# Optimization experiments

Measured on AMD Instinct MI355X. Metric: run time of the kernel, lower is better.

## Reference

```python
import jax, jax.numpy as jnp
import numpy as np

B, S, D, H = 4, 2048, 512, 8
EPS = 1e-5

def _layer_norm(x, gamma, beta):
    mu = jnp.mean(x, axis=-1, keepdims=True)
    var = jnp.mean(jnp.square(x - mu), axis=-1, keepdims=True)
    return (x - mu) * jax.lax.rsqrt(var + EPS) * gamma + beta

def setup_inputs() -> dict:
    key = jax.random.key(0)
    ks = jax.random.split(key, 6)
    sc = 1.0 / np.sqrt(D)
    return {
        "seq_k": jax.random.normal(ks[0], (B, S, D), jnp.float32),
        "seq_q": jax.random.normal(ks[1], (B, S, D), jnp.float32),
        "seq_v": jax.random.normal(ks[2], (B, S, D), jnp.float32),
        "W1": jax.random.normal(ks[3], (D, D), jnp.float32) * sc,
        "W2": jax.random.normal(ks[4], (D, D), jnp.float32) * sc,
        "W3": jax.random.normal(ks[5], (D, D), jnp.float32) * sc,
        "gamma": jnp.ones((D,), jnp.float32),
        "beta": jnp.zeros((D,), jnp.float32),
    }

def reference(seq_k, seq_q, seq_v, W1, W2, W3, gamma, beta):
    # is_layer_norm=True: pre-LN on values; seq_v_value is the normed v
    v_in = _layer_norm(seq_v, gamma, beta)
    # nn.Linear(bias=False): y = x @ W^T
    q = seq_q @ W1.T
    k = seq_k @ W2.T
    v = v_in @ W3.T
    hd = D // H
    q = q.reshape(B, S, H, hd).transpose(0, 2, 1, 3)  # b h s d
    k = k.reshape(B, S, H, hd).transpose(0, 2, 1, 3)
    v = v.reshape(B, S, H, hd).transpose(0, 2, 1, 3)
    # faithful quirk: scores = K @ Q^T, unscaled
    scores = jnp.einsum("bhid,bhjd->bhij", k, q)  # b h s s
    attn = jax.nn.softmax(scores, axis=-1)
    out = jnp.einsum("bhij,bhjd->bhid", attn, v)  # b h s d
    out = out.transpose(0, 2, 1, 3).reshape(B, S, D)
    out = out + v_in                 # is_residual=True
    return _layer_norm(out, gamma, beta)  # final LN
```

## Files before the change

### kernel.cpp

```cpp
#include <hip/hip_runtime.h>
#include <math.h>

#define BB 4
#define SS 2048
#define DD 512
#define HH 8
#define HD 64
#define NTOK (BB*SS)
#define EPS 1e-5f
#define NE ((size_t)NTOK * DD)
#define WN ((size_t)DD * DD)
#define LOG2E 1.4426950408889634f

typedef _Float16 half8v __attribute__((ext_vector_type(8)));
typedef _Float16 half4v __attribute__((ext_vector_type(4)));
typedef _Float16 half2v __attribute__((ext_vector_type(2)));
typedef float f32x4 __attribute__((ext_vector_type(4)));

__device__ __forceinline__ float fast_exp2(float x) {
#if __has_builtin(__builtin_amdgcn_exp2f)
    return __builtin_amdgcn_exp2f(x);
#else
    return __expf(x * 0.6931471805599453f);
#endif
}

__device__ __forceinline__ half2v pack2(float a, float b) {
    return __builtin_bit_cast(half2v, __builtin_amdgcn_cvt_pkrtz(a, b));
}

__device__ __forceinline__ half4v pack4(float a, float b, float c, float d) {
    half2v lo = pack2(a, b);
    half2v hi = pack2(c, d);
    half4v r; r[0] = lo[0]; r[1] = lo[1]; r[2] = hi[0]; r[3] = hi[1];
    return r;
}

__device__ __forceinline__ void gload_lds16(const void* g, void* l) {
    __builtin_amdgcn_global_load_lds(
        (const __attribute__((address_space(1))) unsigned int*)g,
        (__attribute__((address_space(3))) unsigned int*)l, 16, 0, 0);
}

__global__ __launch_bounds__(256) void ln_kernel(const float* __restrict__ x,
                                                 const float* __restrict__ res,
                                                 const float* __restrict__ gamma,
                                                 const float* __restrict__ beta,
                                                 float* __restrict__ y) {
    int row = blockIdx.x;
    const float* xr = x + (size_t)row * DD;
    int t = threadIdx.x;
    float2 v = ((const float2*)xr)[t];
    {
        float2 r = ((const float2*)(res + (size_t)row * DD))[t];
        v.x += r.x; v.y += r.y;
    }
    float s = v.x + v.y;
    float ss = v.x * v.x + v.y * v.y;
    #pragma unroll
    for (int off = 32; off; off >>= 1) {
        s  += __shfl_down(s,  off);
        ss += __shfl_down(ss, off);
    }
    __shared__ float ws0[4], ws1[4];
    int wid = t >> 6, lane = t & 63;
    if (lane == 0) { ws0[wid] = s; ws1[wid] = ss; }
    __syncthreads();
    __shared__ float mu_s, rstd_s;
    if (t == 0) {
        float S0 = ws0[0] + ws0[1] + ws0[2] + ws0[3];
        float S1 = ws1[0] + ws1[1] + ws1[2] + ws1[3];
        float mu = S0 * (1.0f / DD);
        float var = S1 * (1.0f / DD) - mu * mu;
        mu_s = mu;
        rstd_s = rsqrtf(var + EPS);
    }
    __syncthreads();
    float mu = mu_s, rstd = rstd_s;
    float2 g = ((const float2*)gamma)[t];
    float2 bb = ((const float2*)beta)[t];
    float2 o;
    o.x = (v.x - mu) * rstd * g.x + bb.x;
    o.y = (v.y - mu) * rstd * g.y + bb.y;
    ((float2*)(y + (size_t)row * DD))[t] = o;
}

__global__ __launch_bounds__(256) void prep_kernel(const float* __restrict__ seq_v,
                                                   const float* __restrict__ seq_q,
                                                   const float* __restrict__ seq_k,
                                                   const float* __restrict__ W1,
                                                   const float* __restrict__ W2,
                                                   const float* __restrict__ W3,
                                                   const float* __restrict__ gamma,
                                                   const float* __restrict__ beta,
                                                   float* __restrict__ v_in,
                                                   _Float16* __restrict__ v16,
                                                   _Float16* __restrict__ qk16,
                                                   _Float16* __restrict__ w16) {
    int bid = blockIdx.x;
    int t = threadIdx.x;
    if (bid < NTOK) {
        int row = bid;
        float2 v = ((const float2*)(seq_v + (size_t)row * DD))[t];
        float s = v.x + v.y;
        float ss = v.x * v.x + v.y * v.y;
        #pragma unroll
        for (int off = 32; off; off >>= 1) {
            s  += __shfl_down(s,  off);
            ss += __shfl_down(ss, off);
        }
        __shared__ float ws0[4], ws1[4];
        int wid = t >> 6, lane = t & 63;
        if (lane == 0) { ws0[wid] = s; ws1[wid] = ss; }
        __syncthreads();
        __shared__ float mu_s, rstd_s;
        if (t == 0) {
            float S0 = ws0[0] + ws0[1] + ws0[2] + ws0[3];
            float S1 = ws1[0] + ws1[1] + ws1[2] + ws1[3];
            float mu = S0 * (1.0f / DD);
            float var = S1 * (1.0f / DD) - mu * mu;
            mu_s = mu;
            rstd_s = rsqrtf(var + EPS);
        }
        __syncthreads();
        float mu = mu_s, rstd = rstd_s;
        float2 g = ((const float2*)gamma)[t];
        float2 bb = ((const float2*)beta)[t];
        float2 o;
        o.x = (v.x - mu) * rstd * g.x + bb.x;
        o.y = (v.y - mu) * rstd * g.y + bb.y;
        ((float2*)(v_in + (size_t)row * DD))[t] = o;
        *(half2v*)&v16[(size_t)row * DD + 2 * t] = pack2(o.x, o.y);
    } else if (bid < 2 * NTOK) {
        size_t i = ((size_t)(bid - NTOK) * 256 + t) * 4;
        const float* src = (i < NE) ? (seq_q + i) : (seq_k + (i - NE));
        float4 v = *(const float4*)src;
        *(half4v*)(qk16 + i) = pack4(v.x, v.y, v.z, v.w);
    } else {
        size_t i = ((size_t)(bid - 2 * NTOK) * 256 + t) * 4;
        const float* src; float sc;
        if (i < WN)          { src = W1 + i;            sc = LOG2E; }
        else if (i < 2 * WN) { src = W2 + (i - WN);     sc = 1.0f; }
        else                 { src = W3 + (i - 2 * WN); sc = 1.0f; }
        float4 v = *(const float4*)src;
        *(half4v*)(w16 + i) = pack4(v.x * sc, v.y * sc, v.z * sc, v.w * sc);
    }
}

#define GBM 128
#define GBN 128
#define GBK 64
__global__ __launch_bounds__(256) void gemm_mfma(const _Float16* __restrict__ Aall,
                                                 const _Float16* __restrict__ Wall,
                                                 _Float16* __restrict__ Call,
                                                 _Float16* __restrict__ vtOut) {
    __shared__ __align__(16) _Float16 As[GBM * GBK];
    __shared__ __align__(16) _Float16 Ws[GBN * GBK];
    int z = blockIdx.z;
    bool isv = (z == 2);
    const _Float16* A = Aall + (size_t)z * NE;
    const _Float16* W = Wall + (size_t)z * WN;
    int t = threadIdx.x, w = t >> 6, lane = t & 63, q = lane >> 4, ln = lane & 15;
    int lrow = lane >> 3, lseg = lane & 7;
    int m0 = blockIdx.y * GBM, n0 = blockIdx.x * GBN;
    int wm = w & 1, wn = w >> 1;
    f32x4 acc[4][4];
    #pragma unroll
    for (int mt = 0; mt < 4; ++mt)
        #pragma unroll
        for (int nt = 0; nt < 4; ++nt)
            acc[mt][nt] = (f32x4){0.f, 0.f, 0.f, 0.f};

    int gs = lseg ^ lrow;
    for (int k0 = 0; k0 < DD; k0 += GBK) {
        #pragma unroll
        for (int p = 0; p < 4; ++p) {
            int r = w * 32 + p * 8 + lrow;
            gload_lds16(A + (size_t)(m0 + r) * DD + k0 + gs * 8,
                        As + (size_t)(w * 32 + p * 8) * GBK);
            gload_lds16(W + (size_t)(n0 + r) * DD + k0 + gs * 8,
                        Ws + (size_t)(w * 32 + p * 8) * GBK);
        }
        __syncthreads();
        #pragma unroll
        for (int kk = 0; kk < 2; ++kk) {
            int ch = ((4 * kk + q) ^ (ln & 7)) * 8;
            half8v af[4], wf[4];
            #pragma unroll
            for (int mt = 0; mt < 4; ++mt)
                af[mt] = *(half8v*)&As[(wm * 64 + mt * 16 + ln) * GBK + ch];
            #pragma unroll
            for (int nt = 0; nt < 4; ++nt)
                wf[nt] = *(half8v*)&Ws[(wn * 64 + nt * 16 + ln) * GBK + ch];
            if (!isv) {
                #pragma unroll
                for (int mt = 0; mt < 4; ++mt)
                    #pragma unroll
                    for (int nt = 0; nt < 4; ++nt)
                        acc[mt][nt] = __builtin_amdgcn_mfma_f32_16x16x32_f16(
                            wf[nt], af[mt], acc[mt][nt], 0, 0, 0);
            } else {
                #pragma unroll
                for (int mt = 0; mt < 4; ++mt)
                    #pragma unroll
                    for (int nt = 0; nt < 4; ++nt)
                        acc[mt][nt] = __builtin_amdgcn_mfma_f32_16x16x32_f16(
                            af[mt], wf[nt], acc[mt][nt], 0, 0, 0);
            }
        }
        __syncthreads();
    }
    if (!isv) {
        _Float16* C = Call + (size_t)z * NE;
        #pragma unroll
        for (int mt = 0; mt < 4; ++mt) {
            int m = m0 + wm * 64 + mt * 16 + ln;
            int b = m >> 11, s = m & (SS - 1);
            #pragma unroll
            for (int nt = 0; nt < 4; ++nt) {
                int nb = n0 + wn * 64 + nt * 16 + q * 4;
                int h = nb >> 6, d0 = nb & 63;
                half4v pv = pack4(acc[mt][nt][0], acc[mt][nt][1],
                                  acc[mt][nt][2], acc[mt][nt][3]);
                *(half4v*)&C[((size_t)(b * HH + h) * SS + s) * HD + d0] = pv;
            }
        }
    } else {
        #pragma unroll
        for (int mt = 0; mt < 4; ++mt) {
            int mb = m0 + wm * 64 + mt * 16 + q * 4;
            int b = mb >> 11, s0 = mb & (SS - 1);
            #pragma unroll
            for (int nt = 0; nt < 4; ++nt) {
                int n = n0 + wn * 64 + nt * 16 + ln;
                int h = n >> 6, d = n & 63;
                half4v pv = pack4(acc[mt][nt][0], acc[mt][nt][1],
                                  acc[mt][nt][2], acc[mt][nt][3]);
                *(half4v*)&vtOut[((size_t)(b * HH + h) * HD + d) * SS + s0] = pv;
            }
        }
    }
}

#define AI 128
#define AJ 64
__global__ __launch_bounds__(512, 4) void attn_mfma(const _Float16* __restrict__ qh,
                                                    const _Float16* __restrict__ kh,
                                                    const _Float16* __restrict__ vt,
                                                    float* __restrict__ out) {
    __shared__ __align__(16) _Float16 Qt[2][AJ * HD];
    __shared__ __align__(16) _Float16 Vs[2][HD * AJ];
    __shared__ __align__(16) _Float16 Ps[AI * AJ];
    int t = threadIdx.x, w = t >> 6, lane = t & 63, q = lane >> 4, ln = lane & 15;
    int i0 = blockIdx.x * AI;
    int bh = blockIdx.y, b = bh >> 3, h = bh & 7;
    const _Float16* Kb = kh + (size_t)bh * SS * HD;
    const _Float16* Qb = qh + (size_t)bh * SS * HD;
    const _Float16* Vb = vt + (size_t)bh * HD * SS;

    half8v kf[2];
    #pragma unroll
    for (int kk = 0; kk < 2; ++kk)
        kf[kk] = *(const half8v*)&Kb[(size_t)(i0 + w * 16 + ln) * HD + kk * 32 + q * 8];

    f32x4 oacc[4], lacc;
    float m_run = -3.0e38f;
    lacc = (f32x4){0.f, 0.f, 0.f, 0.f};
    #pragma unroll
    for (int mtd = 0; mtd < 4; ++mtd) oacc[mtd] = (f32x4){0.f, 0.f, 0.f, 0.f};
    half8v ones;
    #pragma unroll
    for (int e = 0; e < 8; ++e) ones[e] = (_Float16)1.0f;
    const f32x4 zf = (f32x4){0.f, 0.f, 0.f, 0.f};

    int sr = t >> 3;
    int sc = t & 7;
    int ssw = sc ^ (sr & 7);

    gload_lds16(Qb + (size_t)sr * HD + ssw * 8, &Qt[0][(size_t)w * 512]);
    gload_lds16(Vb + (size_t)sr * SS + ssw * 8, &Vs[0][(size_t)w * 512]);

    const int NITER = SS / AJ;
    for (int jt = 0; jt < NITER; ++jt) {
        int cur = jt & 1;
        __syncthreads();

        if (jt + 1 < NITER) {
            int j1 = (jt + 1) * AJ;
            gload_lds16(Qb + (size_t)(j1 + sr) * HD + ssw * 8, &Qt[cur ^ 1][(size_t)w * 512]);
            gload_lds16(Vb + (size_t)sr * SS + j1 + ssw * 8,   &Vs[cur ^ 1][(size_t)w * 512]);
        }

        f32x4 sacc[4];
        #pragma unroll
        for (int mt = 0; mt < 4; ++mt) {
            half8v qf = *(half8v*)&Qt[cur][(mt * 16 + ln) * HD + (q ^ (ln & 7)) * 8];
            sacc[mt] = __builtin_amdgcn_mfma_f32_16x16x32_f16(qf, kf[0], zf, 0, 0, 0);
        }
        #pragma unroll
        for (int mt = 0; mt < 4; ++mt) {
            half8v qf = *(half8v*)&Qt[cur][(mt * 16 + ln) * HD + ((4 + q) ^ (ln & 7)) * 8];
            sacc[mt] = __builtin_amdgcn_mfma_f32_16x16x32_f16(qf, kf[1], sacc[mt], 0, 0, 0);
        }

        float mx = sacc[0][0];
        #pragma unroll
        for (int mt = 0; mt < 4; ++mt)
            #pragma unroll
            for (int r = 0; r < 4; ++r) mx = fmaxf(mx, sacc[mt][r]);
        mx = fmaxf(mx, __shfl_xor(mx, 16));
        mx = fmaxf(mx, __shfl_xor(mx, 32));
        float mn = fmaxf(m_run, mx);
        if (__any(mn > m_run)) {
            float a = fast_exp2(m_run - mn);
            lacc *= a;
            #pragma unroll
            for (int mtd = 0; mtd < 4; ++mtd) oacc[mtd] *= a;
        }
        m_run = mn;

        int rp = w * 16 + ln;
        #pragma unroll
        for (int mt = 0; mt < 4; ++mt) {
            float p0 = fast_exp2(sacc[mt][0] - mn);
            float p1 = fast_exp2(sacc[mt][1] - mn);
            float p2 = fast_exp2(sacc[mt][2] - mn);
            float p3 = fast_exp2(sacc[mt][3] - mn);
            int cw = mt * 2 + (q >> 1);
            int pos = cw ^ (ln & 7);
            *(half4v*)&Ps[(size_t)rp * AJ + pos * 8 + (q & 1) * 4] =
                pack4(p0, p1, p2, p3);
        }

        #pragma unroll
        for (int ks = 0; ks < 2; ++ks) {
            int pos = ((ks * 4 + q) ^ (ln & 7)) * 8;
            half8v pf = *(half8v*)&Ps[(size_t)(w * 16 + ln) * AJ + pos];
            lacc = __builtin_amdgcn_mfma_f32_16x16x32_f16(ones, pf, lacc, 0, 0, 0);
            #pragma unroll
            for (int mtd = 0; mtd < 4; ++mtd) {
                half8v vf = *(half8v*)&Vs[cur][(size_t)(mtd * 16 + ln) * AJ + pos];
                oacc[mtd] = __builtin_amdgcn_mfma_f32_16x16x32_f16(vf, pf, oacc[mtd], 0, 0, 0);
            }
        }
    }

    float inv = 1.0f / lacc[0];
    int i = i0 + w * 16 + ln;
    #pragma unroll
    for (int mtd = 0; mtd < 4; ++mtd) {
        float4 o;
        o.x = oacc[mtd][0] * inv;
        o.y = oacc[mtd][1] * inv;
        o.z = oacc[mtd][2] * inv;
        o.w = oacc[mtd][3] * inv;
        *(float4*)&out[(size_t)(b * SS + i) * DD + h * HD + mtd * 16 + q * 4] = o;
    }
}

extern "C" void kernel_launch(void* const* d_in, const int* in_sizes, int n_in,
                              void* d_out, int out_size, void* d_ws, size_t ws_size,
                              hipStream_t stream) {
    const float* seq_k = (const float*)d_in[0];
    const float* seq_q = (const float*)d_in[1];
    const float* seq_v = (const float*)d_in[2];
    const float* W1    = (const float*)d_in[3];
    const float* W2    = (const float*)d_in[4];
    const float* W3    = (const float*)d_in[5];
    const float* gamma = (const float*)d_in[6];
    const float* beta  = (const float*)d_in[7];
    float* out = (float*)d_out;

    const size_t MB = 1024 * 1024;
    char* w8 = (char*)d_ws;
    float*    v_in = (float*)w8;
    _Float16* a16  = (_Float16*)(w8 + 16 * MB);
    _Float16* w16  = (_Float16*)(w8 + 40 * MB);
    _Float16* qh   = (_Float16*)(w8 + 48 * MB);
    _Float16* vt   = (_Float16*)(w8 + 64 * MB);
    float*    ao   = (float*)(w8 + 16 * MB);

    _Float16* q16 = a16;
    _Float16* v16 = a16 + 2 * NE;
    _Float16* kh  = qh + NE;

    hipLaunchKernelGGL(prep_kernel, dim3(2 * NTOK + 768), dim3(256), 0, stream,
                       seq_v, seq_q, seq_k, W1, W2, W3, gamma, beta,
                       v_in, v16, q16, w16);
    hipLaunchKernelGGL(gemm_mfma, dim3(DD / GBN, NTOK / GBM, 3), dim3(256), 0, stream,
                       a16, w16, qh, vt);
    hipLaunchKernelGGL(attn_mfma, dim3(SS / AI, BB * HH), dim3(512), 0, stream,
                       qh, kh, vt, ao);
    hipLaunchKernelGGL(ln_kernel, dim3(NTOK), dim3(256), 0, stream,
                       ao, v_in, gamma, beta, out);
}
```

Before: 196.6 us.

## Give each attention wave two query row tiles and defer softmax max rescaling

The attention kernel now runs 4 waves of 256 threads instead of 8, and each wave handles 32 K rows in two 16-row chunks. Every Q and V fragment read from LDS is reused across both chunks, which halves LDS fragment traffic per MFMA. Each thread now issues twice as many global-to-LDS loads per tile. The running max is only updated when the new max exceeds the old one by more than 7 in log2 units, which skips most rescale passes but lets exponentials reach up to 2^7 before normalisation, with some fp16 range risk. s_setprio is raised around the MFMA sections, and register pressure roughly doubles, which may lower occupancy.

```diff
diff --git a/kernel.cpp b/kernel.cpp
--- a/kernel.cpp
+++ b/kernel.cpp
@@ -244,7 +244,7 @@
 
 #define AI 128
 #define AJ 64
-__global__ __launch_bounds__(512, 4) void attn_mfma(const _Float16* __restrict__ qh,
+__global__ __launch_bounds__(256, 2) void attn_mfma(const _Float16* __restrict__ qh,
                                                     const _Float16* __restrict__ kh,
                                                     const _Float16* __restrict__ vt,
                                                     float* __restrict__ out) {
@@ -258,16 +258,22 @@
     const _Float16* Qb = qh + (size_t)bh * SS * HD;
     const _Float16* Vb = vt + (size_t)bh * HD * SS;
 
-    half8v kf[2];
-    #pragma unroll
-    for (int kk = 0; kk < 2; ++kk)
-        kf[kk] = *(const half8v*)&Kb[(size_t)(i0 + w * 16 + ln) * HD + kk * 32 + q * 8];
-
-    f32x4 oacc[4], lacc;
-    float m_run = -3.0e38f;
-    lacc = (f32x4){0.f, 0.f, 0.f, 0.f};
-    #pragma unroll
-    for (int mtd = 0; mtd < 4; ++mtd) oacc[mtd] = (f32x4){0.f, 0.f, 0.f, 0.f};
+    half8v kf[2][2];
+    #pragma unroll
+    for (int c = 0; c < 2; ++c)
+        #pragma unroll
+        for (int kk = 0; kk < 2; ++kk)
+            kf[c][kk] = *(const half8v*)&Kb[(size_t)(i0 + w * 32 + c * 16 + ln) * HD
+                                            + kk * 32 + q * 8];
+
+    f32x4 oacc[2][4], lacc[2];
+    float m_run[2] = {-3.0e38f, -3.0e38f};
+    lacc[0] = (f32x4){0.f, 0.f, 0.f, 0.f};
+    lacc[1] = (f32x4){0.f, 0.f, 0.f, 0.f};
+    #pragma unroll
+    for (int c = 0; c < 2; ++c)
+        #pragma unroll
+        for (int mtd = 0; mtd < 4; ++mtd) oacc[c][mtd] = (f32x4){0.f, 0.f, 0.f, 0.f};
     half8v ones;
     #pragma unroll
     for (int e = 0; e < 8; ++e) ones[e] = (_Float16)1.0f;
@@ -277,8 +283,10 @@
     int sc = t & 7;
     int ssw = sc ^ (sr & 7);
 
-    gload_lds16(Qb + (size_t)sr * HD + ssw * 8, &Qt[0][(size_t)w * 512]);
-    gload_lds16(Vb + (size_t)sr * SS + ssw * 8, &Vs[0][(size_t)w * 512]);
+    gload_lds16(Qb + (size_t)sr * HD + ssw * 8,        &Qt[0][w * 512]);
+    gload_lds16(Qb + (size_t)(sr + 32) * HD + ssw * 8, &Qt[0][2048 + w * 512]);
+    gload_lds16(Vb + (size_t)sr * SS + ssw * 8,        &Vs[0][w * 512]);
+    gload_lds16(Vb + (size_t)(sr + 32) * SS + ssw * 8, &Vs[0][2048 + w * 512]);
 
     const int NITER = SS / AJ;
     for (int jt = 0; jt < NITER; ++jt) {
@@ -287,74 +295,94 @@
 
         if (jt + 1 < NITER) {
             int j1 = (jt + 1) * AJ;
-            gload_lds16(Qb + (size_t)(j1 + sr) * HD + ssw * 8, &Qt[cur ^ 1][(size_t)w * 512]);
-            gload_lds16(Vb + (size_t)sr * SS + j1 + ssw * 8,   &Vs[cur ^ 1][(size_t)w * 512]);
-        }
-
-        f32x4 sacc[4];
+            gload_lds16(Qb + (size_t)(j1 + sr) * HD + ssw * 8,      &Qt[cur ^ 1][w * 512]);
+            gload_lds16(Qb + (size_t)(j1 + sr + 32) * HD + ssw * 8, &Qt[cur ^ 1][2048 + w * 512]);
+            gload_lds16(Vb + (size_t)sr * SS + j1 + ssw * 8,        &Vs[cur ^ 1][w * 512]);
+            gload_lds16(Vb + (size_t)(sr + 32) * SS + j1 + ssw * 8, &Vs[cur ^ 1][2048 + w * 512]);
+        }
+
+        f32x4 sacc[2][4];
+        __builtin_amdgcn_s_setprio(1);
         #pragma unroll
         for (int mt = 0; mt < 4; ++mt) {
             half8v qf = *(half8v*)&Qt[cur][(mt * 16 + ln) * HD + (q ^ (ln & 7)) * 8];
-            sacc[mt] = __builtin_amdgcn_mfma_f32_16x16x32_f16(qf, kf[0], zf, 0, 0, 0);
+            sacc[0][mt] = __builtin_amdgcn_mfma_f32_16x16x32_f16(qf, kf[0][0], zf, 0, 0, 0);
+            sacc[1][mt] = __builtin_amdgcn_mfma_f32_16x16x32_f16(qf, kf[1][0], zf, 0, 0, 0);
         }
         #pragma unroll
         for (int mt = 0; mt < 4; ++mt) {
             half8v qf = *(half8v*)&Qt[cur][(mt * 16 + ln) * HD + ((4 + q) ^ (ln & 7)) * 8];
-            sacc[mt] = __builtin_amdgcn_mfma_f32_16x16x32_f16(qf, kf[1], sacc[mt], 0, 0, 0);
-        }
-
-        float mx = sacc[0][0];
-        #pragma unroll
-        for (int mt = 0; mt < 4; ++mt)
-            #pragma unroll
-            for (int r = 0; r < 4; ++r) mx = fmaxf(mx, sacc[mt][r]);
-        mx = fmaxf(mx, __shfl_xor(mx, 16));
-        mx = fmaxf(mx, __shfl_xor(mx, 32));
-        float mn = fmaxf(m_run, mx);
-        if (__any(mn > m_run)) {
-            float a = fast_exp2(m_run - mn);
-            lacc *= a;
-            #pragma unroll
-            for (int mtd = 0; mtd < 4; ++mtd) oacc[mtd] *= a;
-        }
-        m_run = mn;
-
-        int rp = w * 16 + ln;
-        #pragma unroll
-        for (int mt = 0; mt < 4; ++mt) {
-            float p0 = fast_exp2(sacc[mt][0] - mn);
-            float p1 = fast_exp2(sacc[mt][1] - mn);
-            float p2 = fast_exp2(sacc[mt][2] - mn);
-            float p3 = fast_exp2(sacc[mt][3] - mn);
-            int cw = mt * 2 + (q >> 1);
-            int pos = cw ^ (ln & 7);
-            *(half4v*)&Ps[(size_t)rp * AJ + pos * 8 + (q & 1) * 4] =
-                pack4(p0, p1, p2, p3);
-        }
-
+            sacc[0][mt] = __builtin_amdgcn_mfma_f32_16x16x32_f16(qf, kf[0][1], sacc[0][mt], 0, 0, 0);
+            sacc[1][mt] = __builtin_amdgcn_mfma_f32_16x16x32_f16(qf, kf[1][1], sacc[1][mt], 0, 0, 0);
+        }
+        __builtin_amdgcn_s_setprio(0);
+
+        #pragma unroll
+        for (int c = 0; c < 2; ++c) {
+            float mx = fmaxf(fmaxf(sacc[c][0][0], sacc[c][0][1]),
+                             fmaxf(sacc[c][0][2], sacc[c][0][3]));
+            #pragma unroll
+            for (int mt = 1; mt < 4; ++mt) {
+                float m2 = fmaxf(fmaxf(sacc[c][mt][0], sacc[c][mt][1]),
+                                 fmaxf(sacc[c][mt][2], sacc[c][mt][3]));
+                mx = fmaxf(mx, m2);
+            }
+            mx = fmaxf(mx, __shfl_xor(mx, 16));
+            mx = fmaxf(mx, __shfl_xor(mx, 32));
+            if (__any(mx > m_run[c] + 7.0f)) {
+                float mn = fmaxf(m_run[c], mx);
+                float a = fast_exp2(m_run[c] - mn);
+                lacc[c] *= a;
+                #pragma unroll
+                for (int mtd = 0; mtd < 4; ++mtd) oacc[c][mtd] *= a;
+                m_run[c] = mn;
+            }
+            float mcur = m_run[c];
+            int rp = w * 32 + c * 16 + ln;
+            #pragma unroll
+            for (int mt = 0; mt < 4; ++mt) {
+                float p0 = fast_exp2(sacc[c][mt][0] - mcur);
+                float p1 = fast_exp2(sacc[c][mt][1] - mcur);
+                float p2 = fast_exp2(sacc[c][mt][2] - mcur);
+                float p3 = fast_exp2(sacc[c][mt][3] - mcur);
+                int cw = mt * 2 + (q >> 1);
+                int pos = cw ^ (ln & 7);
+                *(half4v*)&Ps[(size_t)rp * AJ + pos * 8 + (q & 1) * 4] =
+                    pack4(p0, p1, p2, p3);
+            }
+        }
+
+        __builtin_amdgcn_s_setprio(1);
         #pragma unroll
         for (int ks = 0; ks < 2; ++ks) {
             int pos = ((ks * 4 + q) ^ (ln & 7)) * 8;
-            half8v pf = *(half8v*)&Ps[(size_t)(w * 16 + ln) * AJ + pos];
-            lacc = __builtin_amdgcn_mfma_f32_16x16x32_f16(ones, pf, lacc, 0, 0, 0);
+            half8v pf0 = *(half8v*)&Ps[(size_t)(w * 32 + ln) * AJ + pos];
+            half8v pf1 = *(half8v*)&Ps[(size_t)(w * 32 + 16 + ln) * AJ + pos];
+            lacc[0] = __builtin_amdgcn_mfma_f32_16x16x32_f16(ones, pf0, lacc[0], 0, 0, 0);
+            lacc[1] = __builtin_amdgcn_mfma_f32_16x16x32_f16(ones, pf1, lacc[1], 0, 0, 0);
             #pragma unroll
             for (int mtd = 0; mtd < 4; ++mtd) {
                 half8v vf = *(half8v*)&Vs[cur][(size_t)(mtd * 16 + ln) * AJ + pos];
-                oacc[mtd] = __builtin_amdgcn_mfma_f32_16x16x32_f16(vf, pf, oacc[mtd], 0, 0, 0);
-            }
-        }
-    }
-
-    float inv = 1.0f / lacc[0];
-    int i = i0 + w * 16 + ln;
-    #pragma unroll
-    for (int mtd = 0; mtd < 4; ++mtd) {
-        float4 o;
-        o.x = oacc[mtd][0] * inv;
-        o.y = oacc[mtd][1] * inv;
-        o.z = oacc[mtd][2] * inv;
-        o.w = oacc[mtd][3] * inv;
-        *(float4*)&out[(size_t)(b * SS + i) * DD + h * HD + mtd * 16 + q * 4] = o;
+                oacc[0][mtd] = __builtin_amdgcn_mfma_f32_16x16x32_f16(vf, pf0, oacc[0][mtd], 0, 0, 0);
+                oacc[1][mtd] = __builtin_amdgcn_mfma_f32_16x16x32_f16(vf, pf1, oacc[1][mtd], 0, 0, 0);
+            }
+        }
+        __builtin_amdgcn_s_setprio(0);
+    }
+
+    #pragma unroll
+    for (int c = 0; c < 2; ++c) {
+        float inv = 1.0f / lacc[c][0];
+        int i = i0 + w * 32 + c * 16 + ln;
+        #pragma unroll
+        for (int mtd = 0; mtd < 4; ++mtd) {
+            float4 o;
+            o.x = oacc[c][mtd][0] * inv;
+            o.y = oacc[c][mtd][1] * inv;
+            o.z = oacc[c][mtd][2] * inv;
+            o.w = oacc[c][mtd][3] * inv;
+            *(float4*)&out[(size_t)(b * SS + i) * DD + h * HD + mtd * 16 + q * 4] = o;
+        }
     }
 }
 
@@ -389,7 +417,7 @@
                        v_in, v16, q16, w16);
     hipLaunchKernelGGL(gemm_mfma, dim3(DD / GBN, NTOK / GBM, 3), dim3(256), 0, stream,
                        a16, w16, qh, vt);
-    hipLaunchKernelGGL(attn_mfma, dim3(SS / AI, BB * HH), dim3(512), 0, stream,
+    hipLaunchKernelGGL(attn_mfma, dim3(SS / AI, BB * HH), dim3(256), 0, stream,
                        qh, kh, vt, ao);
     hipLaunchKernelGGL(ln_kernel, dim3(NTOK), dim3(256), 0, stream,
                        ao, v_in, gamma, beta, out);
```

Result: slower. 203.5 us (+3.5%).

## Software-pipeline QK^T one tile ahead, lazy max rescale, remap grid to XCDs

Applied to the files above, without the earlier changes.

The attention loop now computes the next tile's scores while the current tile's softmax and PV products run. A third Q LDS buffer lets Q be prefetched two tiles ahead, and s_setprio wraps the MFMA sections. The running-max rescale is skipped unless the new max exceeds the old one by more than 7 in log2 space. The grid is flattened to 1D with a remap meant to place blocks of the same batch-head on the same XCD for L2 reuse. The cost is extra registers for the look-ahead scores and more LDS, and the unbounded p values up to 2^7 risk fp16 range or precision issues.

```diff
diff --git a/kernel.cpp b/kernel.cpp
--- a/kernel.cpp
+++ b/kernel.cpp
@@ -248,12 +248,15 @@
                                                     const _Float16* __restrict__ kh,
                                                     const _Float16* __restrict__ vt,
                                                     float* __restrict__ out) {
-    __shared__ __align__(16) _Float16 Qt[2][AJ * HD];
+    __shared__ __align__(16) _Float16 Qt[3][AJ * HD];
     __shared__ __align__(16) _Float16 Vs[2][HD * AJ];
     __shared__ __align__(16) _Float16 Ps[AI * AJ];
     int t = threadIdx.x, w = t >> 6, lane = t & 63, q = lane >> 4, ln = lane & 15;
-    int i0 = blockIdx.x * AI;
-    int bh = blockIdx.y, b = bh >> 3, h = bh & 7;
+    int wg = blockIdx.x;
+    int slot = wg >> 3;
+    int bh = (wg & 7) * 4 + (slot >> 4);
+    int i0 = (slot & 15) * AI;
+    int b = bh >> 3, h = bh & 7;
     const _Float16* Kb = kh + (size_t)bh * SS * HD;
     const _Float16* Qb = qh + (size_t)bh * SS * HD;
     const _Float16* Vb = vt + (size_t)bh * HD * SS;
@@ -279,59 +282,80 @@
 
     gload_lds16(Qb + (size_t)sr * HD + ssw * 8, &Qt[0][(size_t)w * 512]);
     gload_lds16(Vb + (size_t)sr * SS + ssw * 8, &Vs[0][(size_t)w * 512]);
-
+    __syncthreads();
+    gload_lds16(Qb + (size_t)(AJ + sr) * HD + ssw * 8, &Qt[1][(size_t)w * 512]);
+
+    f32x4 sacc[4];
+    #pragma unroll
+    for (int mt = 0; mt < 4; ++mt) {
+        half8v qf = *(half8v*)&Qt[0][(mt * 16 + ln) * HD + (q ^ (ln & 7)) * 8];
+        sacc[mt] = __builtin_amdgcn_mfma_f32_16x16x32_f16(qf, kf[0], zf, 0, 0, 0);
+    }
+    #pragma unroll
+    for (int mt = 0; mt < 4; ++mt) {
+        half8v qf = *(half8v*)&Qt[0][(mt * 16 + ln) * HD + ((4 + q) ^ (ln & 7)) * 8];
+        sacc[mt] = __builtin_amdgcn_mfma_f32_16x16x32_f16(qf, kf[1], sacc[mt], 0, 0, 0);
+    }
+
+    int rb = 1, sb = 2, vb = 0;
     const int NITER = SS / AJ;
     for (int jt = 0; jt < NITER; ++jt) {
-        int cur = jt & 1;
         __syncthreads();
 
+        if (jt + 2 < NITER)
+            gload_lds16(Qb + (size_t)((jt + 2) * AJ + sr) * HD + ssw * 8,
+                        &Qt[sb][(size_t)w * 512]);
+        if (jt + 1 < NITER)
+            gload_lds16(Vb + (size_t)sr * SS + (jt + 1) * AJ + ssw * 8,
+                        &Vs[vb ^ 1][(size_t)w * 512]);
+
+        f32x4 snx[4] = {zf, zf, zf, zf};
         if (jt + 1 < NITER) {
-            int j1 = (jt + 1) * AJ;
-            gload_lds16(Qb + (size_t)(j1 + sr) * HD + ssw * 8, &Qt[cur ^ 1][(size_t)w * 512]);
-            gload_lds16(Vb + (size_t)sr * SS + j1 + ssw * 8,   &Vs[cur ^ 1][(size_t)w * 512]);
-        }
-
-        f32x4 sacc[4];
-        #pragma unroll
-        for (int mt = 0; mt < 4; ++mt) {
-            half8v qf = *(half8v*)&Qt[cur][(mt * 16 + ln) * HD + (q ^ (ln & 7)) * 8];
-            sacc[mt] = __builtin_amdgcn_mfma_f32_16x16x32_f16(qf, kf[0], zf, 0, 0, 0);
-        }
-        #pragma unroll
-        for (int mt = 0; mt < 4; ++mt) {
-            half8v qf = *(half8v*)&Qt[cur][(mt * 16 + ln) * HD + ((4 + q) ^ (ln & 7)) * 8];
-            sacc[mt] = __builtin_amdgcn_mfma_f32_16x16x32_f16(qf, kf[1], sacc[mt], 0, 0, 0);
-        }
-
-        float mx = sacc[0][0];
-        #pragma unroll
-        for (int mt = 0; mt < 4; ++mt)
-            #pragma unroll
-            for (int r = 0; r < 4; ++r) mx = fmaxf(mx, sacc[mt][r]);
+            __builtin_amdgcn_s_setprio(1);
+            #pragma unroll
+            for (int mt = 0; mt < 4; ++mt) {
+                half8v qf = *(half8v*)&Qt[rb][(mt * 16 + ln) * HD + (q ^ (ln & 7)) * 8];
+                snx[mt] = __builtin_amdgcn_mfma_f32_16x16x32_f16(qf, kf[0], zf, 0, 0, 0);
+            }
+            #pragma unroll
+            for (int mt = 0; mt < 4; ++mt) {
+                half8v qf = *(half8v*)&Qt[rb][(mt * 16 + ln) * HD + ((4 + q) ^ (ln & 7)) * 8];
+                snx[mt] = __builtin_amdgcn_mfma_f32_16x16x32_f16(qf, kf[1], snx[mt], 0, 0, 0);
+            }
+            __builtin_amdgcn_s_setprio(0);
+        }
+
+        float mx = fmaxf(fmaxf(sacc[0][0], sacc[0][1]), fmaxf(sacc[0][2], sacc[0][3]));
+        #pragma unroll
+        for (int mt = 1; mt < 4; ++mt) {
+            float m2 = fmaxf(fmaxf(sacc[mt][0], sacc[mt][1]),
+                             fmaxf(sacc[mt][2], sacc[mt][3]));
+            mx = fmaxf(mx, m2);
+        }
         mx = fmaxf(mx, __shfl_xor(mx, 16));
         mx = fmaxf(mx, __shfl_xor(mx, 32));
-        float mn = fmaxf(m_run, mx);
-        if (__any(mn > m_run)) {
+        if (__any(mx > m_run + 7.0f)) {
+            float mn = fmaxf(m_run, mx);
             float a = fast_exp2(m_run - mn);
             lacc *= a;
             #pragma unroll
             for (int mtd = 0; mtd < 4; ++mtd) oacc[mtd] *= a;
-        }
-        m_run = mn;
-
+            m_run = mn;
+        }
         int rp = w * 16 + ln;
         #pragma unroll
         for (int mt = 0; mt < 4; ++mt) {
-            float p0 = fast_exp2(sacc[mt][0] - mn);
-            float p1 = fast_exp2(sacc[mt][1] - mn);
-            float p2 = fast_exp2(sacc[mt][2] - mn);
-            float p3 = fast_exp2(sacc[mt][3] - mn);
+            float p0 = fast_exp2(sacc[mt][0] - m_run);
+            float p1 = fast_exp2(sacc[mt][1] - m_run);
+            float p2 = fast_exp2(sacc[mt][2] - m_run);
+            float p3 = fast_exp2(sacc[mt][3] - m_run);
             int cw = mt * 2 + (q >> 1);
             int pos = cw ^ (ln & 7);
             *(half4v*)&Ps[(size_t)rp * AJ + pos * 8 + (q & 1) * 4] =
                 pack4(p0, p1, p2, p3);
         }
 
+        __builtin_amdgcn_s_setprio(1);
         #pragma unroll
         for (int ks = 0; ks < 2; ++ks) {
             int pos = ((ks * 4 + q) ^ (ln & 7)) * 8;
@@ -339,10 +363,17 @@
             lacc = __builtin_amdgcn_mfma_f32_16x16x32_f16(ones, pf, lacc, 0, 0, 0);
             #pragma unroll
             for (int mtd = 0; mtd < 4; ++mtd) {
-                half8v vf = *(half8v*)&Vs[cur][(size_t)(mtd * 16 + ln) * AJ + pos];
+                half8v vf = *(half8v*)&Vs[vb][(size_t)(mtd * 16 + ln) * AJ + pos];
                 oacc[mtd] = __builtin_amdgcn_mfma_f32_16x16x32_f16(vf, pf, oacc[mtd], 0, 0, 0);
             }
         }
+        __builtin_amdgcn_s_setprio(0);
+
+        #pragma unroll
+        for (int mt = 0; mt < 4; ++mt) sacc[mt] = snx[mt];
+        rb = (rb == 2) ? 0 : rb + 1;
+        sb = (sb == 2) ? 0 : sb + 1;
+        vb ^= 1;
     }
 
     float inv = 1.0f / lacc[0];
@@ -389,7 +420,7 @@
                        v_in, v16, q16, w16);
     hipLaunchKernelGGL(gemm_mfma, dim3(DD / GBN, NTOK / GBM, 3), dim3(256), 0, stream,
                        a16, w16, qh, vt);
-    hipLaunchKernelGGL(attn_mfma, dim3(SS / AI, BB * HH), dim3(512), 0, stream,
+    hipLaunchKernelGGL(attn_mfma, dim3((SS / AI) * BB * HH), dim3(512), 0, stream,
                        qh, kh, vt, ao);
     hipLaunchKernelGGL(ln_kernel, dim3(NTOK), dim3(256), 0, stream,
                        ao, v_in, gamma, beta, out);
```

New measurement: 201.7 us. +2.6%, slower.
